# Performance work log

Measured on AMD Instinct MI355X. Metric: run time of the kernel, lower is better.

The kernel has to match this reference:

```python
import jax, jax.numpy as jnp
import numpy as np
from jax import lax

EPS = 1e-3  # BatchNorm4d eps


def conv4d(x, w, b):
    """4D conv (VALID, stride 1) via kt-shifted 3D convolutions.
    x: [B, Cin, T, D, H, W]; w: [Cout, Cin, kt, kd, kh, kw]; b: [Cout].
    Returns [B, Cout, T', D', H', W']."""
    B, C, T = x.shape[0], x.shape[1], x.shape[2]
    kt = w.shape[2]
    T_out = T - kt + 1
    acc = 0.0
    for i in range(kt):  # tiny fixed loop over kernel's first spatial dim
        xs = x[:, :, i:i + T_out]                              # [B,C,T_out,D,H,W]
        xs = jnp.transpose(xs, (0, 2, 1, 3, 4, 5))             # [B,T_out,C,D,H,W]
        xs = xs.reshape(B * T_out, C, *x.shape[3:])            # fold T_out into batch
        y = lax.conv_general_dilated(
            xs, w[:, :, i], window_strides=(1, 1, 1), padding='VALID',
            dimension_numbers=('NCDHW', 'OIDHW', 'NCDHW'))
        acc = acc + y                                          # [B*T_out,Cout,D',H',W']
    O = w.shape[0]
    y = acc.reshape(B, T_out, O, *acc.shape[2:])
    y = jnp.transpose(y, (0, 2, 1, 3, 4, 5))                   # [B,Cout,T',D',H',W']
    return y + b[None, :, None, None, None, None]


def setup_inputs() -> dict:
    key = jax.random.key(0)
    k = jax.random.split(key, 7)
    Cin, filters, ks = 4, 3, 3
    Cmid, Cout = Cin * filters, Cin * filters * filters        # 12, 36
    x = jax.random.normal(k[0], (8, Cin, 20, 24, 24, 24), dtype=jnp.float32)
    W1 = jax.random.normal(k[1], (Cmid, Cin, ks, ks, ks, ks), dtype=jnp.float32) * 0.05
    b1 = jax.random.normal(k[2], (Cmid,), dtype=jnp.float32) * 0.05
    gamma = jnp.ones((Cmid,), dtype=jnp.float32)
    beta = jnp.zeros((Cmid,), dtype=jnp.float32)
    W2 = jax.random.normal(k[3], (Cout, Cmid, ks, ks, ks, ks), dtype=jnp.float32) * 0.05
    b2 = jax.random.normal(k[4], (Cout,), dtype=jnp.float32) * 0.05
    return {"x": x, "W1": W1, "b1": b1, "gamma": gamma, "beta": beta,
            "W2": W2, "b2": b2}


def reference(x, W1, b1, gamma, beta, W2, b2):
    h = jax.nn.relu(conv4d(x, W1, b1))                         # conv1 -> ReLU
    # BatchNorm4d (training mode: batch statistics over B and all 4 spatial dims)
    mean = jnp.mean(h, axis=(0, 2, 3, 4, 5), keepdims=True)
    var = jnp.var(h, axis=(0, 2, 3, 4, 5), keepdims=True)
    g = gamma[None, :, None, None, None, None]
    bb = beta[None, :, None, None, None, None]
    h = (h - mean) * jax.lax.rsqrt(var + EPS) * g + bb
    h = jax.nn.relu(conv4d(h, W2, b2))                         # conv2 -> ReLU
    return h.reshape(h.shape[0], -1)                           # flatten
```

## Files before the change

kernel.cpp:

```cpp
#include <hip/hip_runtime.h>

#define EPS 0.001f

typedef __attribute__((ext_vector_type(8))) short bf16x8;
typedef __attribute__((ext_vector_type(4))) short bf16x4;
typedef __attribute__((ext_vector_type(4))) float f32x4;

constexpr int Bn = 8, Tx = 20, Dx = 24, Hx = 24, Wx = 24;
constexpr int Cmid = 12, CoutN = 36;
constexpr int T1 = 18, D1 = 22;
constexpr int T2 = 16, D2 = 20;

constexpr int SXD = 576, SXT = 13824, SXC = 276480;
constexpr long SXB = 1105920;

constexpr int XTD = 2304, XTT = 55296;
constexpr long XTB = (long)Tx * XTT;

constexpr int HTW = 16;
constexpr int HTH = 22 * 16;
constexpr int HTD = 22 * 22 * 16;
constexpr int HTT = 22 * HTD;
constexpr long HTB = (long)T1 * HTT;

constexpr int S2D = 400, S2T = 8000, S2O = 128000;
constexpr long S2B = 4608000;

constexpr int NBLK1 = 8 * 18 * 22;

constexpr int SLAB_B_SZ = 49152;
constexpr int ABUF_OFF  = 2 * SLAB_B_SZ;
constexpr int ABUF_SZ   = 12288;
constexpr int LDS_TOT   = ABUF_OFF + 2 * ABUF_SZ;

__device__ __forceinline__ unsigned short f2bf(float f) {
    unsigned u = __builtin_bit_cast(unsigned, f);
    u = (u + 0x7fffu + ((u >> 16) & 1u)) >> 16;
    return (unsigned short)u;
}

__device__ __forceinline__ void gload16(const void* g, void* l) {
    __builtin_amdgcn_global_load_lds(
        (const __attribute__((address_space(1))) void*)g,
        (__attribute__((address_space(3))) void*)l, 16, 0, 0);
}

template<int N> __device__ __forceinline__ void waitvm() {
    asm volatile("s_waitcnt vmcnt(%0)" :: "i"(N) : "memory");
}

__global__ __launch_bounds__(576) void k_xt(const float* __restrict__ x,
                                            unsigned short* __restrict__ xt) {
    const int tid = threadIdx.x;
    const int d = blockIdx.x, t = blockIdx.y, b = blockIdx.z;
    const float* src = x + (long)b * SXB + (long)t * SXT + (long)d * SXD + tid;
    float v0 = src[0];
    float v1 = src[SXC];
    float v2 = src[2 * SXC];
    float v3 = src[3 * SXC];
    uint2 p;
    p.x = (unsigned)f2bf(v0) | ((unsigned)f2bf(v1) << 16);
    p.y = (unsigned)f2bf(v2) | ((unsigned)f2bf(v3) << 16);
    *(uint2*)(xt + (long)b * XTB + (long)t * XTT + (long)d * XTD + tid * 4) = p;
}

__global__ void k_finW1(const float* __restrict__ W1, unsigned short* __restrict__ Wf1) {
    const int p = blockIdx.x;
    const int lane = threadIdx.x;
    const int m = lane & 15;
    const int q = lane >> 4;
    unsigned short vals[8];
#pragma unroll
    for (int j = 0; j < 8; ++j) {
        int kk = q * 8 + j;
        int g = 2 * p + (kk >> 4);
        int r = kk & 15;
        int kw = r >> 2, cin = r & 3;
        float v = 0.f;
        if (m < 12 && kw < 3 && g < 27) {
            int kt = g / 9, g9 = g - kt * 9, kd = g9 / 3, kh = g9 - kd * 3;
            v = W1[m * 324 + cin * 81 + kt * 27 + kd * 9 + kh * 3 + kw];
        }
        vals[j] = f2bf(v);
    }
    uint4 pk;
    pk.x = (unsigned)vals[0] | ((unsigned)vals[1] << 16);
    pk.y = (unsigned)vals[2] | ((unsigned)vals[3] << 16);
    pk.z = (unsigned)vals[4] | ((unsigned)vals[5] << 16);
    pk.w = (unsigned)vals[6] | ((unsigned)vals[7] << 16);
    *(uint4*)(Wf1 + p * 512 + lane * 8) = pk;
}

__global__ __launch_bounds__(512, 4) void k_conv1m(
    const unsigned short* __restrict__ xt, const unsigned short* __restrict__ Wf1,
    const float* __restrict__ b1, unsigned short* __restrict__ h1t,
    float* __restrict__ part)
{
    __shared__ char lds[9 * 4608 + 16];
    __shared__ float ssum[8][12], ssq[8][12];

    const int tid  = threadIdx.x;
    const int lane = tid & 63;
    const int wv   = tid >> 6;

    const int l  = blockIdx.x;
    const int sw = (l & 7) * 396 + (l >> 3);
    const int d  = sw % 22;
    const int tt = sw / 22;
    const int t  = tt % 18;
    const int b  = tt / 18;
    const int bid = (b * 18 + t) * 22 + d;

    const int n16 = lane & 15;
    const int q   = lane >> 4;

    {
#pragma unroll
        for (int r = 0; r < 5; ++r) {
            int i = r * 512 + tid;
            int p = i / 288, rr = i - p * 288;
            int kt = p / 3, kd = p - kt * 3;
            const unsigned short* src = xt + (long)b * XTB + (long)(t + kt) * XTT
                                      + (long)(d + kd) * XTD + rr * 8;
            gload16(src, lds + (r * 512 + wv * 64) * 16);
        }
        if (tid < 32) {
            int i = 2560 + tid;
            int p = i / 288, rr = i - p * 288;
            int kt = p / 3, kd = p - kt * 3;
            const unsigned short* src = xt + (long)b * XTB + (long)(t + kt) * XTT
                                      + (long)(d + kd) * XTD + rr * 8;
            gload16(src, lds + 2560 * 16);
        }
    }

    bf16x8 A[14];
#pragma unroll
    for (int p = 0; p < 14; ++p)
        A[p] = *(const bf16x8*)(Wf1 + p * 512 + lane * 8);

    int hh[4], ww[4], nn[4];
#pragma unroll
    for (int u = 0; u < 4; ++u) {
        int n = (wv * 4 + u) * 16 + n16;
        nn[u] = n;
        int nc = n < 484 ? n : 483;
        hh[u] = nc / 22;
        ww[u] = nc - hh[u] * 22;
    }

    f32x4 acc[4];
#pragma unroll
    for (int u = 0; u < 4; ++u) acc[u] = (f32x4){0.f, 0.f, 0.f, 0.f};

    __syncthreads();

#pragma unroll
    for (int p = 0; p < 14; ++p) {
        int gq = 2 * p + (q >> 1);
        int gc = gq < 27 ? gq : 26;
        int kt = gc / 9, g9 = gc - kt * 9, kd = g9 / 3, kh = g9 - kd * 3;
        const int off = (kt * 3 + kd) * 4608 + kh * 192 + (q & 1) * 16;
#pragma unroll
        for (int u = 0; u < 4; ++u) {
            const int addr = off + hh[u] * 192 + ww[u] * 8;
            bf16x4 lo = *(const bf16x4*)(lds + addr);
            bf16x4 hi = *(const bf16x4*)(lds + addr + 8);
            bf16x8 bb;
            bb[0] = lo[0]; bb[1] = lo[1]; bb[2] = lo[2]; bb[3] = lo[3];
            bb[4] = hi[0]; bb[5] = hi[1]; bb[6] = hi[2]; bb[7] = hi[3];
            acc[u] = __builtin_amdgcn_mfma_f32_16x16x32_bf16(A[p], bb, acc[u], 0, 0, 0);
        }
    }

    const int c0 = q * 4;
    float bias[4];
#pragma unroll
    for (int r = 0; r < 4; ++r) bias[r] = (c0 + r) < 12 ? b1[c0 + r] : 0.f;

    float ls[4] = {0.f, 0.f, 0.f, 0.f}, lq[4] = {0.f, 0.f, 0.f, 0.f};
#pragma unroll
    for (int u = 0; u < 4; ++u) {
        const bool valid = nn[u] < 484;
        float v[4];
#pragma unroll
        for (int r = 0; r < 4; ++r) {
            float val = fmaxf(acc[u][r] + bias[r], 0.f);
            v[r] = val;
            if (valid) { ls[r] += val; lq[r] += val * val; }
        }
        if (valid) {
            const long ob = (long)b * HTB + (long)t * HTT + (long)d * HTD
                          + (long)hh[u] * HTH + (long)ww[u] * HTW + c0;
            uint2 pk;
            pk.x = (unsigned)f2bf(v[0]) | ((unsigned)f2bf(v[1]) << 16);
            pk.y = (unsigned)f2bf(v[2]) | ((unsigned)f2bf(v[3]) << 16);
            *(uint2*)(h1t + ob) = pk;
        }
    }

#pragma unroll
    for (int off = 8; off > 0; off >>= 1) {
#pragma unroll
        for (int r = 0; r < 4; ++r) {
            ls[r] += __shfl_xor(ls[r], off);
            lq[r] += __shfl_xor(lq[r], off);
        }
    }
    if (n16 == 0 && q < 3) {
#pragma unroll
        for (int r = 0; r < 4; ++r) {
            ssum[wv][c0 + r] = ls[r];
            ssq[wv][c0 + r] = lq[r];
        }
    }
    __syncthreads();
    if (tid < 12) {
        float s = 0.f;
#pragma unroll
        for (int i = 0; i < 8; ++i) s += ssum[i][tid];
        part[tid * NBLK1 + bid] = s;
    } else if (tid < 24) {
        float s = 0.f;
#pragma unroll
        for (int i = 0; i < 8; ++i) s += ssq[i][tid - 12];
        part[tid * NBLK1 + bid] = s;
    }
}

__global__ void k_red(const float* __restrict__ part, float* __restrict__ stats2) {
    __shared__ float s[256];
    const int c = blockIdx.x;
    const int tid = threadIdx.x;
    float acc = 0.f;
    for (int i = tid; i < NBLK1; i += 256) acc += part[c * NBLK1 + i];
    s[tid] = acc;
    __syncthreads();
    for (int off = 128; off > 0; off >>= 1) {
        if (tid < off) s[tid] += s[tid + off];
        __syncthreads();
    }
    if (tid == 0) stats2[c] = s[0];
}

__global__ void k_fin1(const float* __restrict__ stats2, const float* __restrict__ gamma,
                       const float* __restrict__ beta, const float* __restrict__ W2,
                       const float* __restrict__ b2, float* __restrict__ abuf,
                       float* __restrict__ b2ws)
{
    __shared__ float d_s[12];
    __shared__ float red[36][12];
    const int tid = threadIdx.x;
    if (tid < 12) {
        const float N = 1533312.f;
        float mean = stats2[tid] / N;
        float var  = stats2[12 + tid] / N - mean * mean;
        float a = gamma[tid] * rsqrtf(var + EPS);
        abuf[tid] = a;
        d_s[tid] = beta[tid] - mean * a;
    }
    __syncthreads();
    if (tid < 432) {
        const int o = tid / 12, c = tid - o * 12;
        const float* p = W2 + o * 972 + c * 81;
        float ts = 0.f;
#pragma unroll
        for (int k = 0; k < 81; ++k) ts += p[k];
        red[o][c] = d_s[c] * ts;
    }
    __syncthreads();
    if (tid < 36) {
        float s = b2[tid];
#pragma unroll
        for (int c = 0; c < 12; ++c) s += red[tid][c];
        b2ws[tid] = s;
    }
}

__global__ void k_fin2(const float* __restrict__ W2, const float* __restrict__ abuf,
                       unsigned short* __restrict__ Wf)
{
    const int bi = blockIdx.x;
    const int lane = threadIdx.x;
    const int ch = bi & 1;
    const int tmp = bi >> 1;
    const int mt = tmp % 3;
    const int g = tmp / 3;
    const int kt = g / 9, g9 = g % 9, kd = g9 / 3, kh = g9 % 3;
    const int o = mt * 16 + (lane & 15);

    unsigned short vals[8];
#pragma unroll
    for (int j = 0; j < 8; ++j) {
        int k = ch * 32 + ((lane >> 4) << 3) + j;
        float v = 0.f;
        if (k < 48 && o < 36) {
            int kw = k >> 4, c = k & 15;
            if (c < 12)
                v = W2[o * 972 + c * 81 + kt * 27 + kd * 9 + kh * 3 + kw] * abuf[c];
        }
        vals[j] = f2bf(v);
    }
    uint4 pk;
    pk.x = (unsigned)vals[0] | ((unsigned)vals[1] << 16);
    pk.y = (unsigned)vals[2] | ((unsigned)vals[3] << 16);
    pk.z = (unsigned)vals[4] | ((unsigned)vals[5] << 16);
    pk.w = (unsigned)vals[6] | ((unsigned)vals[7] << 16);
    *(uint4*)(Wf + bi * 512 + lane * 8) = pk;
}

__global__ __launch_bounds__(512, 2) void k_conv2m(
    const unsigned short* __restrict__ h1t, const unsigned short* __restrict__ Wf,
    const float* __restrict__ b2ws, float* __restrict__ out)
{
    __shared__ char lds[LDS_TOT];

    const int tid  = threadIdx.x;
    const int lane = tid & 63;
    const int wv   = tid >> 6;

    const int l   = blockIdx.x;
    const int b   = l & 7;
    const int rem = l >> 3;
    const int d   = rem % 20;
    const int t0  = (rem / 20) * 2;

    const int n16 = lane & 15;
    const int q   = lane >> 4;

    auto stage_slab = [&](int ktIn, int buf) {
        const unsigned short* base = h1t + (long)b * HTB + (long)(t0 + ktIn) * HTT
                                   + (long)d * HTD;
#pragma unroll
        for (int r = 0; r < 6; ++r) {
            int j = r * 512 + wv * 64 + lane;
            int f = ((j % 44) >> 3) & 1;
            gload16(base + (long)(j ^ f) * 8,
                    lds + buf * SLAB_B_SZ + (r * 512 + wv * 64) * 16);
        }
    };
    auto stage_A = [&](int tt) {
        const int dstb = ABUF_OFF + (tt & 1) * ABUF_SZ;
#pragma unroll
        for (int r = 0; r < 2; ++r) {
            int j  = wv * 96 + r * 32 + lane;
            int fi = j >> 6;
            int sl = j & 63;
            int pe = fi / 6;
            int r6 = fi - pe * 6;
            int mt = r6 >> 1, ch = r6 & 1;
            int gA = tt - pe * 9;
            gA = (gA >= 0 && gA < 27) ? gA : 0;
            int idx = (gA * 3 + mt) * 2 + ch;
            gload16(Wf + idx * 512 + sl * 8,
                    lds + dstb + (wv * 96 + r * 32) * 16);
        }
    };

    int rb0a[4], rb1a[4], pba[4];
    bool val[4];
#pragma unroll
    for (int ps = 0; ps < 4; ++ps) {
        int pt = ps * 8 + wv;
        val[ps] = pt < 25;
        int ptc = val[ps] ? pt : 0;
        int n = ptc * 16 + n16;
        int h = n / 20, w = n - h * 20;
        pba[ps] = n;
        int posb = n / 20 * 704 + w * 32;
        int u0 = 2 * w + q;
        int u1 = 2 * w + 4 + (q & 1);
        rb0a[ps] = (posb + q * 16) ^ (((u0 >> 3) & 1) << 4);
        rb1a[ps] = (posb + (q & 1) * 16 + 64) ^ (((u1 >> 3) & 1) << 4);
        (void)h;
    }

    f32x4 acc[4][2][3];
#pragma unroll
    for (int ps = 0; ps < 4; ++ps)
#pragma unroll
        for (int pe = 0; pe < 2; ++pe)
#pragma unroll
            for (int mt = 0; mt < 3; ++mt)
                acc[ps][pe][mt] = (f32x4){0.f, 0.f, 0.f, 0.f};

    stage_slab(0, 0);
    stage_A(0);

#define COMPUTE_STEP(KT, G9V, PE0, PE1)                                          \
  {                                                                              \
    const int g9_ = (G9V);                                                       \
    const int kd_ = g9_ / 3, kh_ = g9_ - kd_ * 3;                                \
    const int goff_ = kd_ * 15488 + kh_ * 704;                                   \
    const char* sbp_ = lds + ((KT) & 1) * SLAB_B_SZ;                             \
    const char* abp_ = lds + ABUF_OFF + (((KT) * 9 + g9_) & 1) * ABUF_SZ;        \
    bf16x8 Af0_[3][2], Af1_[3][2];                                               \
    if (PE0) {                                                                   \
      _Pragma("unroll") for (int mt = 0; mt < 3; ++mt)                           \
        _Pragma("unroll") for (int ch = 0; ch < 2; ++ch)                         \
          Af0_[mt][ch] = *(const bf16x8*)(abp_ + (mt * 2 + ch) * 1024 + lane * 16); \
    }                                                                            \
    if (PE1) {                                                                   \
      _Pragma("unroll") for (int mt = 0; mt < 3; ++mt)                           \
        _Pragma("unroll") for (int ch = 0; ch < 2; ++ch)                         \
          Af1_[mt][ch] = *(const bf16x8*)(abp_ + (6 + mt * 2 + ch) * 1024 + lane * 16); \
    }                                                                            \
    __builtin_amdgcn_s_setprio(1);                                               \
    _Pragma("unroll")                                                            \
    for (int ps = 0; ps < 4; ++ps) if (val[ps]) {                                \
      bf16x8 b0_ = *(const bf16x8*)(sbp_ + rb0a[ps] + goff_);                    \
      bf16x8 b1_ = *(const bf16x8*)(sbp_ + rb1a[ps] + goff_);                    \
      if (PE0) {                                                                 \
        _Pragma("unroll") for (int mt = 0; mt < 3; ++mt) {                       \
          acc[ps][0][mt] = __builtin_amdgcn_mfma_f32_16x16x32_bf16(Af0_[mt][0], b0_, acc[ps][0][mt], 0, 0, 0); \
          acc[ps][0][mt] = __builtin_amdgcn_mfma_f32_16x16x32_bf16(Af0_[mt][1], b1_, acc[ps][0][mt], 0, 0, 0); \
        }                                                                        \
      }                                                                          \
      if (PE1) {                                                                 \
        _Pragma("unroll") for (int mt = 0; mt < 3; ++mt) {                       \
          acc[ps][1][mt] = __builtin_amdgcn_mfma_f32_16x16x32_bf16(Af1_[mt][0], b0_, acc[ps][1][mt], 0, 0, 0); \
          acc[ps][1][mt] = __builtin_amdgcn_mfma_f32_16x16x32_bf16(Af1_[mt][1], b1_, acc[ps][1][mt], 0, 0, 0); \
        }                                                                        \
      }                                                                          \
    }                                                                            \
    __builtin_amdgcn_s_setprio(0);                                               \
  }

#define FULL_STEP(KT, G9V, VMN, DOSLAB)                                          \
  {                                                                              \
    const int s_ = (KT) * 9 + (G9V);                                             \
    if (s_ < 35) stage_A(s_ + 1);                                                \
    if (DOSLAB) stage_slab((KT) + 1, ((KT) + 1) & 1);                            \
    waitvm<VMN>();                                                               \
    __builtin_amdgcn_s_barrier();                                                \
    __builtin_amdgcn_sched_barrier(0);                                           \
    COMPUTE_STEP(KT, G9V, ((KT) < 3), ((KT) > 0))                                \
    __builtin_amdgcn_s_barrier();                                                \
  }

    for (int g9 = 0; g9 < 4; ++g9) FULL_STEP(0, g9, 2, false)
    FULL_STEP(0, 4, 8, true)
    FULL_STEP(0, 5, 8, false)
    for (int g9 = 6; g9 < 9; ++g9) FULL_STEP(0, g9, 2, false)
    for (int g9 = 0; g9 < 4; ++g9) FULL_STEP(1, g9, 2, false)
    FULL_STEP(1, 4, 8, true)
    FULL_STEP(1, 5, 8, false)
    for (int g9 = 6; g9 < 9; ++g9) FULL_STEP(1, g9, 2, false)
    for (int g9 = 0; g9 < 4; ++g9) FULL_STEP(2, g9, 2, false)
    FULL_STEP(2, 4, 8, true)
    FULL_STEP(2, 5, 8, false)
    for (int g9 = 6; g9 < 9; ++g9) FULL_STEP(2, g9, 2, false)
    for (int g9 = 0; g9 < 8; ++g9) FULL_STEP(3, g9, 2, false)
    FULL_STEP(3, 8, 0, false)

#undef FULL_STEP
#undef COMPUTE_STEP

    const long obase = (long)b * S2B + (long)d * S2D;
#pragma unroll
    for (int ps = 0; ps < 4; ++ps) if (val[ps]) {
#pragma unroll
        for (int pe = 0; pe < 2; ++pe) {
            const long ot = obase + (long)(t0 + pe) * S2T;
#pragma unroll
            for (int mt = 0; mt < 3; ++mt)
#pragma unroll
            for (int r = 0; r < 4; ++r) {
                const int o = mt * 16 + q * 4 + r;
                if (o < 36)
                    out[ot + (long)o * S2O + pba[ps]] =
                        fmaxf(acc[ps][pe][mt][r] + b2ws[o], 0.f);
            }
        }
    }
}

extern "C" void kernel_launch(void* const* d_in, const int* in_sizes, int n_in,
                              void* d_out, int out_size, void* d_ws, size_t ws_size,
                              hipStream_t stream) {
    const float* x     = (const float*)d_in[0];
    const float* W1    = (const float*)d_in[1];
    const float* b1    = (const float*)d_in[2];
    const float* gamma = (const float*)d_in[3];
    const float* beta  = (const float*)d_in[4];
    const float* W2    = (const float*)d_in[5];
    const float* b2    = (const float*)d_in[6];
    float* out = (float*)d_out;

    float* ws     = (float*)d_ws;
    float* stats2 = ws;
    float* abuf   = ws + 32;
    float* b2ws   = ws + 64;
    unsigned short* Wf1 = (unsigned short*)((char*)d_ws + 1024);
    unsigned short* Wf  = (unsigned short*)((char*)d_ws + 16384);
    float* part   = (float*)((char*)d_ws + 196608);
    unsigned short* h1t = (unsigned short*)((char*)d_ws + 524288);
    unsigned short* xt  = (unsigned short*)((char*)d_ws + 50331648);

    k_xt<<<dim3(24, 20, 8), 576, 0, stream>>>(x, xt);
    k_finW1<<<14, 64, 0, stream>>>(W1, Wf1);
    k_conv1m<<<3168, 512, 0, stream>>>(xt, Wf1, b1, h1t, part);
    k_red<<<24, 256, 0, stream>>>(part, stats2);
    k_fin1<<<1, 512, 0, stream>>>(stats2, gamma, beta, W2, b2, abuf, b2ws);
    k_fin2<<<162, 64, 0, stream>>>(W2, abuf, Wf);
    k_conv2m<<<1280, 512, 0, stream>>>(h1t, Wf, b2ws, out);
}
```

Before: 420.5 us.

## Process two kernel taps per barrier step and prefetch slabs earlier

The conv2 main loop now stages weight fragments for two taps at once, with a doubled A buffer, so each barrier pair covers two compute steps. This halves the number of block-wide barriers and waits. The first two input slabs are loaded up front and later slabs are issued at fixed steps with adjusted vmcnt waits. The cost is more LDS per block, which may reduce occupancy, and the compute is now a runtime loop instead of fully unrolled macros.

```diff
diff --git a/kernel.cpp b/kernel.cpp
--- a/kernel.cpp
+++ b/kernel.cpp
@@ -30,7 +30,7 @@
 
 constexpr int SLAB_B_SZ = 49152;
 constexpr int ABUF_OFF  = 2 * SLAB_B_SZ;
-constexpr int ABUF_SZ   = 12288;
+constexpr int ABUF_SZ   = 24576;
 constexpr int LDS_TOT   = ABUF_OFF + 2 * ABUF_SZ;
 
 __device__ __forceinline__ unsigned short f2bf(float f) {
@@ -328,8 +328,8 @@
     const int n16 = lane & 15;
     const int q   = lane >> 4;
 
-    auto stage_slab = [&](int ktIn, int buf) {
-        const unsigned short* base = h1t + (long)b * HTB + (long)(t0 + ktIn) * HTT
+    auto stage_slab = [&](int t_in, int buf) {
+        const unsigned short* base = h1t + (long)b * HTB + (long)t_in * HTT
                                    + (long)d * HTD;
 #pragma unroll
         for (int r = 0; r < 6; ++r) {
@@ -339,21 +339,19 @@
                     lds + buf * SLAB_B_SZ + (r * 512 + wv * 64) * 16);
         }
     };
-    auto stage_A = [&](int tt) {
-        const int dstb = ABUF_OFF + (tt & 1) * ABUF_SZ;
-#pragma unroll
-        for (int r = 0; r < 2; ++r) {
-            int j  = wv * 96 + r * 32 + lane;
-            int fi = j >> 6;
-            int sl = j & 63;
-            int pe = fi / 6;
-            int r6 = fi - pe * 6;
-            int mt = r6 >> 1, ch = r6 & 1;
-            int gA = tt - pe * 9;
+    auto stage_A2 = [&](int ss) {
+        const int dstb = ABUF_OFF + (ss & 1) * ABUF_SZ;
+#pragma unroll
+        for (int r = 0; r < 3; ++r) {
+            int frag = wv * 3 + r;
+            int e   = frag / 12, r12 = frag - e * 12;
+            int pe  = r12 / 6,   r6  = r12 - pe * 6;
+            int mt  = r6 >> 1,   ch  = r6 & 1;
+            int ttv = 2 * ss + e;
+            int gA  = ttv - pe * 9;
             gA = (gA >= 0 && gA < 27) ? gA : 0;
             int idx = (gA * 3 + mt) * 2 + ch;
-            gload16(Wf + idx * 512 + sl * 8,
-                    lds + dstb + (wv * 96 + r * 32) * 16);
+            gload16(Wf + idx * 512 + lane * 8, lds + dstb + frag * 1024);
         }
     };
 
@@ -367,12 +365,11 @@
         int n = ptc * 16 + n16;
         int h = n / 20, w = n - h * 20;
         pba[ps] = n;
-        int posb = n / 20 * 704 + w * 32;
+        int posb = h * 704 + w * 32;
         int u0 = 2 * w + q;
         int u1 = 2 * w + 4 + (q & 1);
         rb0a[ps] = (posb + q * 16) ^ (((u0 >> 3) & 1) << 4);
         rb1a[ps] = (posb + (q & 1) * 16 + 64) ^ (((u1 >> 3) & 1) << 4);
-        (void)h;
     }
 
     f32x4 acc[4][2][3];
@@ -384,77 +381,72 @@
             for (int mt = 0; mt < 3; ++mt)
                 acc[ps][pe][mt] = (f32x4){0.f, 0.f, 0.f, 0.f};
 
-    stage_slab(0, 0);
-    stage_A(0);
-
-#define COMPUTE_STEP(KT, G9V, PE0, PE1)                                          \
-  {                                                                              \
-    const int g9_ = (G9V);                                                       \
-    const int kd_ = g9_ / 3, kh_ = g9_ - kd_ * 3;                                \
-    const int goff_ = kd_ * 15488 + kh_ * 704;                                   \
-    const char* sbp_ = lds + ((KT) & 1) * SLAB_B_SZ;                             \
-    const char* abp_ = lds + ABUF_OFF + (((KT) * 9 + g9_) & 1) * ABUF_SZ;        \
-    bf16x8 Af0_[3][2], Af1_[3][2];                                               \
-    if (PE0) {                                                                   \
-      _Pragma("unroll") for (int mt = 0; mt < 3; ++mt)                           \
-        _Pragma("unroll") for (int ch = 0; ch < 2; ++ch)                         \
-          Af0_[mt][ch] = *(const bf16x8*)(abp_ + (mt * 2 + ch) * 1024 + lane * 16); \
-    }                                                                            \
-    if (PE1) {                                                                   \
-      _Pragma("unroll") for (int mt = 0; mt < 3; ++mt)                           \
-        _Pragma("unroll") for (int ch = 0; ch < 2; ++ch)                         \
-          Af1_[mt][ch] = *(const bf16x8*)(abp_ + (6 + mt * 2 + ch) * 1024 + lane * 16); \
-    }                                                                            \
-    __builtin_amdgcn_s_setprio(1);                                               \
-    _Pragma("unroll")                                                            \
-    for (int ps = 0; ps < 4; ++ps) if (val[ps]) {                                \
-      bf16x8 b0_ = *(const bf16x8*)(sbp_ + rb0a[ps] + goff_);                    \
-      bf16x8 b1_ = *(const bf16x8*)(sbp_ + rb1a[ps] + goff_);                    \
-      if (PE0) {                                                                 \
-        _Pragma("unroll") for (int mt = 0; mt < 3; ++mt) {                       \
-          acc[ps][0][mt] = __builtin_amdgcn_mfma_f32_16x16x32_bf16(Af0_[mt][0], b0_, acc[ps][0][mt], 0, 0, 0); \
-          acc[ps][0][mt] = __builtin_amdgcn_mfma_f32_16x16x32_bf16(Af0_[mt][1], b1_, acc[ps][0][mt], 0, 0, 0); \
-        }                                                                        \
-      }                                                                          \
-      if (PE1) {                                                                 \
-        _Pragma("unroll") for (int mt = 0; mt < 3; ++mt) {                       \
-          acc[ps][1][mt] = __builtin_amdgcn_mfma_f32_16x16x32_bf16(Af1_[mt][0], b0_, acc[ps][1][mt], 0, 0, 0); \
-          acc[ps][1][mt] = __builtin_amdgcn_mfma_f32_16x16x32_bf16(Af1_[mt][1], b1_, acc[ps][1][mt], 0, 0, 0); \
-        }                                                                        \
-      }                                                                          \
-    }                                                                            \
-    __builtin_amdgcn_s_setprio(0);                                               \
-  }
-
-#define FULL_STEP(KT, G9V, VMN, DOSLAB)                                          \
-  {                                                                              \
-    const int s_ = (KT) * 9 + (G9V);                                             \
-    if (s_ < 35) stage_A(s_ + 1);                                                \
-    if (DOSLAB) stage_slab((KT) + 1, ((KT) + 1) & 1);                            \
-    waitvm<VMN>();                                                               \
-    __builtin_amdgcn_s_barrier();                                                \
-    __builtin_amdgcn_sched_barrier(0);                                           \
-    COMPUTE_STEP(KT, G9V, ((KT) < 3), ((KT) > 0))                                \
-    __builtin_amdgcn_s_barrier();                                                \
-  }
-
-    for (int g9 = 0; g9 < 4; ++g9) FULL_STEP(0, g9, 2, false)
-    FULL_STEP(0, 4, 8, true)
-    FULL_STEP(0, 5, 8, false)
-    for (int g9 = 6; g9 < 9; ++g9) FULL_STEP(0, g9, 2, false)
-    for (int g9 = 0; g9 < 4; ++g9) FULL_STEP(1, g9, 2, false)
-    FULL_STEP(1, 4, 8, true)
-    FULL_STEP(1, 5, 8, false)
-    for (int g9 = 6; g9 < 9; ++g9) FULL_STEP(1, g9, 2, false)
-    for (int g9 = 0; g9 < 4; ++g9) FULL_STEP(2, g9, 2, false)
-    FULL_STEP(2, 4, 8, true)
-    FULL_STEP(2, 5, 8, false)
-    for (int g9 = 6; g9 < 9; ++g9) FULL_STEP(2, g9, 2, false)
-    for (int g9 = 0; g9 < 8; ++g9) FULL_STEP(3, g9, 2, false)
-    FULL_STEP(3, 8, 0, false)
-
-#undef FULL_STEP
-#undef COMPUTE_STEP
+    auto compute_tt = [&](int ttv, const char* abp_e) {
+        const int KT = ttv / 9;
+        const int g9 = ttv - KT * 9;
+        const int kd = g9 / 3, kh = g9 - kd * 3;
+        const int goff = kd * 15488 + kh * 704;
+        const char* sbp = lds + (KT & 1) * SLAB_B_SZ;
+        const bool PE0 = (ttv < 27), PE1 = (ttv >= 9);
+        bf16x8 Af0[3][2], Af1[3][2];
+        if (PE0) {
+#pragma unroll
+            for (int mt = 0; mt < 3; ++mt)
+#pragma unroll
+                for (int ch = 0; ch < 2; ++ch)
+                    Af0[mt][ch] = *(const bf16x8*)(abp_e + (mt * 2 + ch) * 1024 + lane * 16);
+        }
+        if (PE1) {
+#pragma unroll
+            for (int mt = 0; mt < 3; ++mt)
+#pragma unroll
+                for (int ch = 0; ch < 2; ++ch)
+                    Af1[mt][ch] = *(const bf16x8*)(abp_e + (6 + mt * 2 + ch) * 1024 + lane * 16);
+        }
+        __builtin_amdgcn_s_setprio(1);
+#pragma unroll
+        for (int ps = 0; ps < 4; ++ps) if (val[ps]) {
+            bf16x8 b0 = *(const bf16x8*)(sbp + rb0a[ps] + goff);
+            bf16x8 b1 = *(const bf16x8*)(sbp + rb1a[ps] + goff);
+            if (PE0) {
+#pragma unroll
+                for (int mt = 0; mt < 3; ++mt) {
+                    acc[ps][0][mt] = __builtin_amdgcn_mfma_f32_16x16x32_bf16(Af0[mt][0], b0, acc[ps][0][mt], 0, 0, 0);
+                    acc[ps][0][mt] = __builtin_amdgcn_mfma_f32_16x16x32_bf16(Af0[mt][1], b1, acc[ps][0][mt], 0, 0, 0);
+                }
+            }
+            if (PE1) {
+#pragma unroll
+                for (int mt = 0; mt < 3; ++mt) {
+                    acc[ps][1][mt] = __builtin_amdgcn_mfma_f32_16x16x32_bf16(Af1[mt][0], b0, acc[ps][1][mt], 0, 0, 0);
+                    acc[ps][1][mt] = __builtin_amdgcn_mfma_f32_16x16x32_bf16(Af1[mt][1], b1, acc[ps][1][mt], 0, 0, 0);
+                }
+            }
+        }
+        __builtin_amdgcn_s_setprio(0);
+    };
+
+    stage_slab(t0 + 0, 0);
+    stage_slab(t0 + 1, 1);
+    stage_A2(0);
+
+    for (int s = 0; s < 18; ++s) {
+        if (s < 17) stage_A2(s + 1);
+        if (s == 5) stage_slab(t0 + 2, 0);
+        if (s == 9) stage_slab(t0 + 3, 1);
+
+        if (s == 17)                               waitvm<0>();
+        else if (s == 5 || s == 6 || s == 9 || s == 10) waitvm<9>();
+        else                                       waitvm<3>();
+        __builtin_amdgcn_s_barrier();
+        __builtin_amdgcn_sched_barrier(0);
+
+        const char* abp = lds + ABUF_OFF + (s & 1) * ABUF_SZ;
+        compute_tt(2 * s,     abp);
+        compute_tt(2 * s + 1, abp + 12288);
+
+        __builtin_amdgcn_s_barrier();
+    }
 
     const long obase = (long)b * S2B + (long)d * S2D;
 #pragma unroll
```

After: 419.9 us. No clear change (-0.1%).
